# Kernel optimization log

Measured on AMD Instinct MI355X. Metric: run time of the kernel, lower is better.

Reference implementation:

```python
import jax, jax.numpy as jnp
import numpy as np
import itertools

VOXEL_SIZE = np.array([0.05, 0.05, 0.1], np.float32)   # xyz, from cfg.voxel_size
GRID_OFFSET = np.array([0.0, -40.0, -3.0], np.float32)  # xyz, cfg.grid_bounds[:3]
BN_EPS = 1e-3

# ---------------- rulebook construction (numpy, mirrors spconv indice pairs) ----------------

def _enc(c, shape):
    Z, Y, X = shape
    c = c.astype(np.int64)
    return ((c[:, 0] * Z + c[:, 1]) * Y + c[:, 2]) * X + c[:, 3]

def _lookup(sk, order, q):
    pos = np.clip(np.searchsorted(sk, q), 0, len(sk) - 1)
    return np.where((q >= 0) & (sk[pos] == q), order[pos], -1).astype(np.int32)

def _subm_rulebook(coords, shape):
    # submanifold conv k=3, pad=1: output sites == input sites; neighbor = out + (k-1)
    keys = _enc(coords, shape)
    order = np.argsort(keys).astype(np.int32)
    sk = keys[order]
    dims = np.array(shape)
    rows = []
    for off in itertools.product((-1, 0, 1), repeat=3):
        nb = coords[:, 1:] + np.array(off)
        inb = ((nb >= 0) & (nb < dims)).all(1)
        full = np.concatenate([coords[:, :1], nb], 1)
        q = np.where(inb, _enc(full, shape), -1)
        rows.append(_lookup(sk, order, q))
    return np.stack(rows)  # [27, N] input index or -1

def _strided_rulebook(coords, shape_in, ksize, stride, pad):
    # regular sparse conv: out active = any site receiving a contribution; in = out*s - p + k
    ksize = np.array(ksize); stride = np.array(stride); pad = np.array(pad)
    shape_out = tuple((((np.array(shape_in) + 2 * pad - ksize) // stride) + 1).tolist())
    keys = _enc(coords, shape_in)
    order = np.argsort(keys).astype(np.int32)
    sk = keys[order]
    cand = []
    for k in itertools.product(*[range(int(x)) for x in ksize]):
        num = coords[:, 1:] + pad - np.array(k)
        ok = (num % stride == 0).all(1)
        o = num // stride
        ok &= (o >= 0).all(1) & (o < np.array(shape_out)).all(1)
        cand.append(np.concatenate([coords[ok, :1], o[ok]], 1))
    out_coords = np.unique(np.concatenate(cand, 0), axis=0).astype(np.int32)
    dims_in = np.array(shape_in)
    rows = []
    for k in itertools.product(*[range(int(x)) for x in ksize]):
        ic = out_coords[:, 1:] * stride - pad + np.array(k)
        inb = ((ic >= 0) & (ic < dims_in)).all(1)
        full = np.concatenate([out_coords[:, :1], ic], 1)
        q = np.where(inb, _enc(full, shape_in), -1)
        rows.append(_lookup(sk, order, q))
    return out_coords, np.stack(rows), shape_out

# ---------------- inputs ----------------

def setup_inputs() -> dict:
    rng = np.random.default_rng(0)
    B, NPB = 2, 8000
    shape0 = (41, 1600, 1280)
    parts = []
    for b in range(B):
        c = np.stack([rng.integers(0, shape0[0], 4 * NPB),
                      rng.integers(0, shape0[1], 4 * NPB),
                      rng.integers(0, shape0[2], 4 * NPB)], 1)
        c = np.unique(c, axis=0)[:NPB]
        parts.append(np.concatenate([np.full((len(c), 1), b), c], 1))
    coords0 = np.concatenate(parts, 0).astype(np.int32)

    rb0 = _subm_rulebook(coords0, shape0)
    coords1, rbc1, shape1 = _strided_rulebook(coords0, shape0, (3, 3, 3), (2, 2, 2), (1, 1, 1))
    rb1 = _subm_rulebook(coords1, shape1)
    coords2, rbc2, shape2 = _strided_rulebook(coords1, shape1, (3, 3, 3), (2, 2, 2), (1, 1, 1))
    rb2 = _subm_rulebook(coords2, shape2)
    coords3, rbc3, shape3 = _strided_rulebook(coords2, shape2, (3, 3, 3), (2, 2, 2), (0, 1, 1))
    rb3 = _subm_rulebook(coords3, shape3)
    coords4, rbc4, shape4 = _strided_rulebook(coords3, shape3, (3, 1, 1), (2, 1, 1), (0, 0, 0))

    def w(*s):
        return jnp.asarray((rng.standard_normal(s) * 0.1).astype(np.float32))

    inp = {"features": jnp.asarray(rng.standard_normal((len(coords0), 4)).astype(np.float32))}
    specs = [("1a", 27, 4, 16), ("1b", 27, 16, 16), ("1c", 27, 16, 32),
             ("2a", 27, 32, 32), ("2b", 27, 32, 32), ("2c", 27, 32, 64),
             ("3a", 27, 64, 64), ("3b", 27, 64, 64), ("3c", 27, 64, 64), ("3d", 27, 64, 64),
             ("4a", 27, 64, 64), ("4b", 27, 64, 64), ("4c", 27, 64, 64), ("4d", 3, 64, 64)]
    for name, K, ci, co in specs:
        inp["w" + name] = w(K, ci, co)
        inp["g" + name] = jnp.asarray((np.abs(rng.standard_normal(co)) + 0.5).astype(np.float32))
        inp["b" + name] = jnp.asarray((rng.standard_normal(co) * 0.1).astype(np.float32))
    inp.update(coordinates=jnp.asarray(coords0), coords1=jnp.asarray(coords1),
               coords2=jnp.asarray(coords2), coords3=jnp.asarray(coords3),
               rb0=jnp.asarray(rb0), rbc1=jnp.asarray(rbc1), rb1=jnp.asarray(rb1),
               rbc2=jnp.asarray(rbc2), rb2=jnp.asarray(rb2), rbc3=jnp.asarray(rbc3),
               rb3=jnp.asarray(rb3), rbc4=jnp.asarray(rbc4), batch_size=B)
    return inp

# ---------------- forward math ----------------

def _sconv(feat, rb, W):
    # gather-GEMM-scatter: rb[k,n] = input row feeding output n via kernel offset k (-1 = none)
    out = jnp.zeros((rb.shape[1], W.shape[2]), feat.dtype)
    for k in range(W.shape[0]):
        idx = rb[k]
        g = jnp.where(idx[:, None] >= 0, feat[jnp.clip(idx, 0)], 0.0)
        out = out + g @ W[k]
    return out

def _bn_relu(x, g, b):
    # BatchNorm1d in training mode over active voxels (biased var), eps=1e-3, then ReLU
    m = jnp.mean(x, 0)
    v = jnp.mean(jnp.square(x - m), 0)
    return jax.nn.relu((x - m) * (g / jnp.sqrt(v + BN_EPS)) + b)

def reference(features, w1a, g1a, b1a, w1b, g1b, b1b, w1c, g1c, b1c,
              w2a, g2a, b2a, w2b, g2b, b2b, w2c, g2c, b2c,
              w3a, g3a, b3a, w3b, g3b, b3b, w3c, g3c, b3c, w3d, g3d, b3d,
              w4a, g4a, b4a, w4b, g4b, b4b, w4c, g4c, b4c, w4d, g4d, b4d,
              coordinates, coords1, coords2, coords3,
              rb0, rbc1, rb1, rbc2, rb2, rbc3, rb3, rbc4, batch_size):
    f0 = features
    h = _bn_relu(_sconv(f0, rb0, w1a), g1a, b1a)
    h = _bn_relu(_sconv(h, rb0, w1b), g1b, b1b)
    f1 = _bn_relu(_sconv(h, rbc1, w1c), g1c, b1c)
    h = _bn_relu(_sconv(f1, rb1, w2a), g2a, b2a)
    h = _bn_relu(_sconv(h, rb1, w2b), g2b, b2b)
    f2 = _bn_relu(_sconv(h, rbc2, w2c), g2c, b2c)
    h = _bn_relu(_sconv(f2, rb2, w3a), g3a, b3a)
    h = _bn_relu(_sconv(h, rb2, w3b), g3b, b3b)
    h = _bn_relu(_sconv(h, rb2, w3c), g3c, b3c)
    f3 = _bn_relu(_sconv(h, rbc3, w3d), g3d, b3d)
    h = _bn_relu(_sconv(f3, rb3, w4a), g4a, b4a)
    h = _bn_relu(_sconv(h, rb3, w4b), g4b, b4b)
    h = _bn_relu(_sconv(h, rb3, w4c), g4c, b4c)
    f4 = _bn_relu(_sconv(h, rbc4, w4d), g4d, b4d)

    vs = jnp.asarray(VOXEL_SIZE)
    off = jnp.asarray(GRID_OFFSET)
    def to_global(stride, c):
        # indices are (b,z,y,x); flip -> (x,y,z,b); take xyz
        return jnp.flip(c, 1)[:, :3].astype(jnp.float32) * (vs * stride) + off
    xyz0 = to_global(1, coordinates)
    xyz1 = to_global(2, coords1)
    xyz2 = to_global(4, coords2)
    xyz3 = to_global(8, coords3)
    return (xyz0, f0, xyz1, f1, xyz2, f2, xyz3, f3, f4)
```

## Files before the change

### kernel.cpp

```cpp
#include <hip/hip_runtime.h>

#define BN_EPS 1e-3f
#define NREP 16

typedef __attribute__((ext_vector_type(8))) short short8;
typedef __attribute__((ext_vector_type(4))) float float4v;

__device__ __forceinline__ short f2bf(float f) {
    unsigned u = __float_as_uint(f);
    unsigned r = (u + 0x7FFFu + ((u >> 16) & 1u)) >> 16;
    return (short)r;
}

template <int N>
__device__ __forceinline__ void waitcnt_vm() {
    __builtin_amdgcn_s_waitcnt(0xF70 | (N & 15) | ((N >> 4) << 14));
}

__device__ __forceinline__ void wave_barrier() { asm volatile("s_barrier" ::: "memory"); }

__device__ __forceinline__ void dma16(const short* g, short* l) {
    __builtin_amdgcn_global_load_lds((const __attribute__((address_space(1))) void*)g,
                                     (__attribute__((address_space(3))) void*)l, 16, 0, 0);
}


__global__ __launch_bounds__(256) void zero_kernel(float* p, int n) {
    int i = blockIdx.x * 256 + threadIdx.x;
    if (i < n) p[i] = 0.f;
}

__global__ __launch_bounds__(256) void copy_kernel(const float* __restrict__ in,
                                                   float* __restrict__ out, int n) {
    int i = blockIdx.x * 256 + threadIdx.x;
    if (i < n) out[i] = in[i];
}

__global__ __launch_bounds__(256) void zero_rows_kernel(short* a, short* b, long maxN) {
    int t = threadIdx.x;
    if (t < 32) a[maxN * 32 + t] = 0;
    else if (t < 96) a[maxN * 64 + (t - 32)] = 0;
    else if (t < 128) b[maxN * 32 + (t - 96)] = 0;
    else if (t < 192) b[maxN * 64 + (t - 128)] = 0;
}

__global__ __launch_bounds__(256) void xyz_kernel(const int* __restrict__ coords,
                                                  float* __restrict__ out, int N,
                                                  float sx, float sy, float sz) {
    int n = blockIdx.x * 256 + threadIdx.x;
    if (n >= N) return;
    int4 c = ((const int4*)coords)[n];
    out[n * 3 + 0] = c.w * sx;
    out[n * 3 + 1] = c.z * sy - 40.0f;
    out[n * 3 + 2] = c.y * sz - 3.0f;
}

__global__ __launch_bounds__(256) void convert_f0(const float* __restrict__ f,
                                                  short* __restrict__ dst, int N) {
    int i = blockIdx.x * 256 + threadIdx.x;
    if (i >= N * 32) return;
    int c = i & 31, n = i >> 5;
    dst[i] = (c < 4) ? f2bf(f[n * 4 + c]) : (short)0;
}

struct PrepAll {
    const float* src[14];
    short* dst[14];
    int CI[14];
    int CO[14];
    int CHP[14];
    int cum[15];
};

__global__ __launch_bounds__(256) void prep_all_kernel(PrepAll d) {
    int i = blockIdx.x * 256 + threadIdx.x;
    if (i >= d.cum[14]) return;
    int l = 0;
    while (l < 13 && i >= d.cum[l + 1]) ++l;
    int f = i - d.cum[l];
    int CO = d.CO[l], CI = d.CI[l];
    int NCH = d.CHP[l] / 32, CT = CO / 16;
    int e = f & 7;
    int u = f >> 3;
    int l16 = u & 15;
    int q = (u >> 4) & 3;
    int u2 = u >> 6;
    int t = u2 % CT;
    int c = (u2 / CT) % NCH;
    int k = u2 / (CT * NCH);
    int ci = c * 32 + q * 8 + e;
    int co = t * 16 + l16;
    float v = (ci < CI) ? d.src[l][((size_t)k * CI + ci) * CO + co] : 0.f;
    d.dst[l][f] = f2bf(v);
}

struct ASet {
    short8 v0, v1, v2, v3;
};

template <int CHP, int CO, int K>
__global__ __launch_bounds__(256, 4) void sconv_hyb(const short* __restrict__ feat,
                                                    const int* __restrict__ rb,
                                                    const short* __restrict__ Wt,
                                                    float* __restrict__ out,
                                                    float* __restrict__ stats, int N, int zrow) {
    constexpr int NCH = CHP / 32;
    constexpr int CT = CO / 16;
    constexpr int BTILE = CO * CHP;
    constexpr int NB = BTILE / 512;
    constexpr int A = 2 * NCH;
    constexpr int ROWS = 128;

    __shared__ __align__(16) short ldsB[3 * BTILE];
    __shared__ int sIdx[K * ROWS];
    __shared__ int sFlag[K];
    __shared__ int sKl[K];
    __shared__ int sKn;

    const int tid = threadIdx.x;
    const int w = tid >> 6;
    const int lane = tid & 63;
    const int quad = lane >> 4;
    const int l16 = lane & 15;
    const int m0 = blockIdx.x * ROWS;

    if (tid < K) sFlag[tid] = 0;
    __syncthreads();
    for (int e = tid; e < K * ROWS; e += 256) {
        int r = m0 + (e & (ROWS - 1));
        int v = (r < N) ? rb[(size_t)(e >> 7) * N + r] : -1;
        sIdx[e] = v;
        if (v >= 0) sFlag[e >> 7] = 1;
    }
    __syncthreads();
    if (w == 0) {
        int f = (lane < K) ? sFlag[lane] : 0;
        unsigned long long m = __ballot(f != 0);
        if (f) sKl[__popcll(m & ((1ull << lane) - 1ull))] = lane;
        if (lane == 0) sKn = (int)__popcll(m);
    }
    __syncthreads();
    const int nk = sKn;

    const short* fquad = feat + quad * 8;

    auto issueB = [&](int kp, int slot) {
        const short* wk = Wt + (size_t)kp * BTILE + lane * 8;
        short* bb = ldsB + slot * BTILE;
#pragma unroll
        for (int jj = 0; jj < (NB + 3) / 4; ++jj) {
            int j = jj * 4 + w;
            if (j < NB) dma16(wk + j * 512, bb + j * 512);
        }
    };
    auto issueA = [&](int kp) {
        ASet s;
        int i0 = sIdx[kp * ROWS + w * 32 + l16];
        int i1 = sIdx[kp * ROWS + w * 32 + 16 + l16];
        const short* p0 = fquad + (size_t)(i0 < 0 ? zrow : i0) * CHP;
        const short* p1 = fquad + (size_t)(i1 < 0 ? zrow : i1) * CHP;
        s.v0 = *(const short8*)p0;
        s.v2 = *(const short8*)p1;
        if constexpr (NCH == 2) {
            s.v1 = *(const short8*)(p0 + 32);
            s.v3 = *(const short8*)(p1 + 32);
        } else {
            s.v1 = (short8)0;
            s.v3 = (short8)0;
        }
        return s;
    };

    float4v acc[2][CT];
#pragma unroll
    for (int mt = 0; mt < 2; ++mt)
#pragma unroll
        for (int t = 0; t < CT; ++t) acc[mt][t] = (float4v)0.f;

    constexpr int BW0 = NB / 4 + ((NB % 4) > 0 ? 1 : 0);
    constexpr int BW1 = NB / 4 + ((NB % 4) > 1 ? 1 : 0);
    constexpr int BW2 = NB / 4 + ((NB % 4) > 2 ? 1 : 0);
    constexpr int BW3 = NB / 4;

    ASet sA{}, sB{}, sC{};
    if (nk > 0) {
        issueB(sKl[0], 0);
        sA = issueA(sKl[0]);
    }
    if (nk > 1) {
        issueB(sKl[1], 1);
        sB = issueA(sKl[1]);
    }

    int slotRd = 0, slotWr = 2;
    for (int i = 0; i < nk; ++i) {
        if (i < nk - 1) {
            if (w == 0) waitcnt_vm<BW0 + A>();
            else if (w == 1) waitcnt_vm<BW1 + A>();
            else if (w == 2) waitcnt_vm<BW2 + A>();
            else waitcnt_vm<BW3 + A>();
        } else {
            waitcnt_vm<0>();
        }
        __builtin_amdgcn_sched_barrier(0);
        wave_barrier();
        if (i + 2 < nk) {
            issueB(sKl[i + 2], slotWr);
            sC = issueA(sKl[i + 2]);
        }
        const short* bb = ldsB + slotRd * BTILE;
#pragma unroll
        for (int c = 0; c < NCH; ++c) {
#pragma unroll
            for (int t = 0; t < CT; ++t) {
                short8 bf = *(const short8*)(bb + ((c * CT + t) * 64 + quad * 16 + l16) * 8);
#pragma unroll
                for (int mt = 0; mt < 2; ++mt) {
                    short8 af = (mt == 0) ? ((c == 0) ? sA.v0 : sA.v1)
                                          : ((c == 0) ? sA.v2 : sA.v3);
                    acc[mt][t] = __builtin_amdgcn_mfma_f32_16x16x32_bf16(af, bf, acc[mt][t], 0,
                                                                         0, 0);
                }
            }
        }
        sA = sB;
        sB = sC;
        slotRd = (slotRd == 2) ? 0 : slotRd + 1;
        slotWr = (slotWr == 2) ? 0 : slotWr + 1;
    }

#pragma unroll
    for (int mt = 0; mt < 2; ++mt)
#pragma unroll
        for (int t = 0; t < CT; ++t) {
            int col = t * 16 + l16;
#pragma unroll
            for (int r = 0; r < 4; ++r) {
                int orow = m0 + w * 32 + mt * 16 + quad * 4 + r;
                if (orow < N) out[(size_t)orow * CO + col] = acc[mt][t][r];
            }
        }

    __syncthreads();
    float* red = (float*)ldsB;
#pragma unroll
    for (int t = 0; t < CT; ++t) {
        float s = 0.f, ss = 0.f;
#pragma unroll
        for (int mt = 0; mt < 2; ++mt)
#pragma unroll
            for (int r = 0; r < 4; ++r) {
                float v = acc[mt][t][r];
                s += v;
                ss += v * v;
            }
        s += __shfl_xor(s, 16);
        s += __shfl_xor(s, 32);
        ss += __shfl_xor(ss, 16);
        ss += __shfl_xor(ss, 32);
        if (lane < 16) {
            red[w * 2 * CO + t * 16 + lane] = s;
            red[w * 2 * CO + CO + t * 16 + lane] = ss;
        }
    }
    __syncthreads();
    if (tid < 2 * CO) {
        float v = red[tid] + red[2 * CO + tid] + red[4 * CO + tid] + red[6 * CO + tid];
        float* st = stats + (size_t)(blockIdx.x & (NREP - 1)) * 128;
        atomicAdd(&st[(tid < CO) ? tid : (64 + tid - CO)], v);
    }
}

template <int COUT, int CHPN, bool F32OUT, bool BFOUT>
__global__ __launch_bounds__(256) void bn_apply(const float* __restrict__ x,
                                                const float* __restrict__ stats,
                                                const float* __restrict__ g,
                                                const float* __restrict__ b,
                                                float* __restrict__ fout,
                                                short* __restrict__ bfout, int N) {
    constexpr int CW = BFOUT ? CHPN : COUT;
    __shared__ float ssc[COUT];
    __shared__ float ssh[COUT];
    int tid = threadIdx.x;
    if (tid < COUT) {
        float s = 0.f, q = 0.f;
#pragma unroll
        for (int r = 0; r < NREP; ++r) {
            s += stats[r * 128 + tid];
            q += stats[r * 128 + 64 + tid];
        }
        float inv = 1.0f / (float)N;
        float m = s * inv;
        float v = q * inv - m * m;
        float sc = g[tid] / sqrtf(v + BN_EPS);
        ssc[tid] = sc;
        ssh[tid] = b[tid] - m * sc;
    }
    __syncthreads();
    long i = (long)blockIdx.x * 256 + tid;
    if (i >= (long)N * CW) return;
    int c = (int)(i % CW);
    long n = i / CW;
    float y = 0.f;
    if (c < COUT) {
        y = fmaxf(x[n * COUT + c] * ssc[c] + ssh[c], 0.f);
        if (F32OUT) __builtin_nontemporal_store(y, &fout[n * COUT + c]);
    }
    if (BFOUT) bfout[n * CHPN + c] = f2bf(y);
}


template <int CHP, int CO, int K>
static void conv(const short* fin, const int* rb, const short* wt, float* preact, float* stats,
                 int N, int zrow, hipStream_t stream) {
    dim3 grid((N + 127) / 128);
    hipLaunchKernelGGL((sconv_hyb<CHP, CO, K>), grid, dim3(256), 0, stream, fin, rb, wt, preact,
                       stats, N, zrow);
}

template <int COUT, int CHPN, bool F32OUT, bool BFOUT>
static void apply(const float* preact, const float* stats, const float* g, const float* b,
                  float* fout, short* bfout, int N, hipStream_t stream) {
    constexpr int CW = BFOUT ? CHPN : COUT;
    int blocks = (int)(((long)N * CW + 255) / 256);
    hipLaunchKernelGGL((bn_apply<COUT, CHPN, F32OUT, BFOUT>), dim3(blocks), dim3(256), 0, stream,
                       preact, stats, g, b, fout, bfout, N);
}

extern "C" void kernel_launch(void* const* d_in, const int* in_sizes, int n_in, void* d_out,
                              int out_size, void* d_ws, size_t ws_size, hipStream_t stream) {
    const float* features = (const float*)d_in[0];
    const float* W[14];
    const float* G[14];
    const float* Bb[14];
    for (int i = 0; i < 14; ++i) {
        W[i] = (const float*)d_in[1 + 3 * i];
        G[i] = (const float*)d_in[2 + 3 * i];
        Bb[i] = (const float*)d_in[3 + 3 * i];
    }
    const int* coords0 = (const int*)d_in[43];
    const int* coords1 = (const int*)d_in[44];
    const int* coords2 = (const int*)d_in[45];
    const int* coords3 = (const int*)d_in[46];
    const int* rb0 = (const int*)d_in[47];
    const int* rbc1 = (const int*)d_in[48];
    const int* rb1 = (const int*)d_in[49];
    const int* rbc2 = (const int*)d_in[50];
    const int* rb2 = (const int*)d_in[51];
    const int* rbc3 = (const int*)d_in[52];
    const int* rb3 = (const int*)d_in[53];
    const int* rbc4 = (const int*)d_in[54];

    const int N0 = in_sizes[0] / 4;
    const int N1 = in_sizes[44] / 4;
    const int N2 = in_sizes[45] / 4;
    const int N3 = in_sizes[46] / 4;
    const int N4 = in_sizes[54] / 3;

    float* out = (float*)d_out;
    long off = 0;
    float* xyz0 = out + off; off += (long)N0 * 3;
    float* f0   = out + off; off += (long)N0 * 4;
    float* xyz1 = out + off; off += (long)N1 * 3;
    float* f1   = out + off; off += (long)N1 * 32;
    float* xyz2 = out + off; off += (long)N2 * 3;
    float* f2   = out + off; off += (long)N2 * 64;
    float* xyz3 = out + off; off += (long)N3 * 3;
    float* f3   = out + off; off += (long)N3 * 64;
    float* f4   = out + off;

    long maxN = N0;
    if (N1 > maxN) maxN = N1;
    if (N2 > maxN) maxN = N2;
    if (N3 > maxN) maxN = N3;
    if (N4 > maxN) maxN = N4;
    const int zrow = (int)maxN;

    float* preact = (float*)d_ws;
    float* statsBase = preact + (size_t)maxN * 64;
    short* bfA = (short*)(statsBase + 14 * NREP * 128);
    short* bfB = bfA + (size_t)(maxN + 1) * 64;
    short* wtBase = bfB + (size_t)(maxN + 1) * 64;

    static const int KK[14] = {27, 27, 27, 27, 27, 27, 27, 27, 27, 27, 27, 27, 27, 3};
    static const int CI[14] = {4, 16, 16, 32, 32, 32, 64, 64, 64, 64, 64, 64, 64, 64};
    static const int CO[14] = {16, 16, 32, 32, 32, 64, 64, 64, 64, 64, 64, 64, 64, 64};
    short* WT[14];
    PrepAll pd;
    {
        size_t o = 0;
        int cum = 0;
        for (int l = 0; l < 14; ++l) {
            WT[l] = wtBase + o;
            int chp = CI[l] <= 32 ? 32 : 64;
            pd.src[l] = W[l];
            pd.dst[l] = WT[l];
            pd.CI[l] = CI[l];
            pd.CO[l] = CO[l];
            pd.CHP[l] = chp;
            pd.cum[l] = cum;
            cum += KK[l] * CO[l] * chp;
            o += (size_t)KK[l] * CO[l] * chp;
        }
        pd.cum[14] = cum;
    }

    int nstats = 14 * NREP * 128;
    hipLaunchKernelGGL(zero_kernel, dim3((nstats + 255) / 256), dim3(256), 0, stream, statsBase,
                       nstats);
    hipLaunchKernelGGL(zero_rows_kernel, dim3(1), dim3(256), 0, stream, bfA, bfB, maxN);
    hipLaunchKernelGGL(prep_all_kernel, dim3((pd.cum[14] + 255) / 256), dim3(256), 0, stream, pd);

    hipLaunchKernelGGL(copy_kernel, dim3((N0 * 4 + 255) / 256), dim3(256), 0, stream, features, f0,
                       N0 * 4);
    hipLaunchKernelGGL(xyz_kernel, dim3((N0 + 255) / 256), dim3(256), 0, stream, coords0, xyz0, N0,
                       0.05f, 0.05f, 0.1f);
    hipLaunchKernelGGL(xyz_kernel, dim3((N1 + 255) / 256), dim3(256), 0, stream, coords1, xyz1, N1,
                       0.1f, 0.1f, 0.2f);
    hipLaunchKernelGGL(xyz_kernel, dim3((N2 + 255) / 256), dim3(256), 0, stream, coords2, xyz2, N2,
                       0.2f, 0.2f, 0.4f);
    hipLaunchKernelGGL(xyz_kernel, dim3((N3 + 255) / 256), dim3(256), 0, stream, coords3, xyz3, N3,
                       0.4f, 0.4f, 0.8f);
    hipLaunchKernelGGL(convert_f0, dim3((N0 * 32 + 255) / 256), dim3(256), 0, stream, features,
                       bfA, N0);

    float* st = statsBase;
#define STAT(l) (st + (size_t)(l)*NREP * 128)

    conv<32, 16, 27>(bfA, rb0, WT[0], preact, STAT(0), N0, zrow, stream);
    apply<16, 32, false, true>(preact, STAT(0), G[0], Bb[0], nullptr, bfB, N0, stream);
    conv<32, 16, 27>(bfB, rb0, WT[1], preact, STAT(1), N0, zrow, stream);
    apply<16, 32, false, true>(preact, STAT(1), G[1], Bb[1], nullptr, bfA, N0, stream);
    conv<32, 32, 27>(bfA, rbc1, WT[2], preact, STAT(2), N1, zrow, stream);
    apply<32, 32, true, true>(preact, STAT(2), G[2], Bb[2], f1, bfB, N1, stream);

    conv<32, 32, 27>(bfB, rb1, WT[3], preact, STAT(3), N1, zrow, stream);
    apply<32, 32, false, true>(preact, STAT(3), G[3], Bb[3], nullptr, bfA, N1, stream);
    conv<32, 32, 27>(bfA, rb1, WT[4], preact, STAT(4), N1, zrow, stream);
    apply<32, 32, false, true>(preact, STAT(4), G[4], Bb[4], nullptr, bfB, N1, stream);
    conv<32, 64, 27>(bfB, rbc2, WT[5], preact, STAT(5), N2, zrow, stream);
    apply<64, 64, true, true>(preact, STAT(5), G[5], Bb[5], f2, bfA, N2, stream);

    conv<64, 64, 27>(bfA, rb2, WT[6], preact, STAT(6), N2, zrow, stream);
    apply<64, 64, false, true>(preact, STAT(6), G[6], Bb[6], nullptr, bfB, N2, stream);
    conv<64, 64, 27>(bfB, rb2, WT[7], preact, STAT(7), N2, zrow, stream);
    apply<64, 64, false, true>(preact, STAT(7), G[7], Bb[7], nullptr, bfA, N2, stream);
    conv<64, 64, 27>(bfA, rb2, WT[8], preact, STAT(8), N2, zrow, stream);
    apply<64, 64, false, true>(preact, STAT(8), G[8], Bb[8], nullptr, bfB, N2, stream);
    conv<64, 64, 27>(bfB, rbc3, WT[9], preact, STAT(9), N3, zrow, stream);
    apply<64, 64, true, true>(preact, STAT(9), G[9], Bb[9], f3, bfA, N3, stream);

    conv<64, 64, 27>(bfA, rb3, WT[10], preact, STAT(10), N3, zrow, stream);
    apply<64, 64, false, true>(preact, STAT(10), G[10], Bb[10], nullptr, bfB, N3, stream);
    conv<64, 64, 27>(bfB, rb3, WT[11], preact, STAT(11), N3, zrow, stream);
    apply<64, 64, false, true>(preact, STAT(11), G[11], Bb[11], nullptr, bfA, N3, stream);
    conv<64, 64, 27>(bfA, rb3, WT[12], preact, STAT(12), N3, zrow, stream);
    apply<64, 64, false, true>(preact, STAT(12), G[12], Bb[12], nullptr, bfB, N3, stream);
    conv<64, 64, 3>(bfB, rbc4, WT[13], preact, STAT(13), N4, zrow, stream);
    apply<64, 64, true, false>(preact, STAT(13), G[13], Bb[13], f4, nullptr, N4, stream);
#undef STAT
}
```

Before: 733.1 us.

## Split sparse conv kernel offsets across grid y and reduce partials separately

The conv kernel now splits the 27 kernel offsets into 4 groups using blockIdx.y. Each group writes its own partial output buffer. A new reduce_stats kernel sums the partials into a combined buffer and computes the BN sum and sum-of-squares statistics, which the conv epilogue no longer does. This raises parallelism for small-N layers and lowers per-block LDS index storage, but it adds extra global memory traffic for the partials, an extra launch per layer, and more reloading of the same rows.

```diff
diff --git a/kernel.cpp b/kernel.cpp
--- a/kernel.cpp
+++ b/kernel.cpp
@@ -98,12 +98,12 @@
     short8 v0, v1, v2, v3;
 };
 
-template <int CHP, int CO, int K>
+template <int CHP, int CO, int KS>
 __global__ __launch_bounds__(256, 4) void sconv_hyb(const short* __restrict__ feat,
                                                     const int* __restrict__ rb,
                                                     const short* __restrict__ Wt,
-                                                    float* __restrict__ out,
-                                                    float* __restrict__ stats, int N, int zrow) {
+                                                    float* __restrict__ parts, long pstride,
+                                                    int N, int zrow, int Ktot) {
     constexpr int NCH = CHP / 32;
     constexpr int CT = CO / 16;
     constexpr int BTILE = CO * CHP;
@@ -112,9 +112,9 @@
     constexpr int ROWS = 128;
 
     __shared__ __align__(16) short ldsB[3 * BTILE];
-    __shared__ int sIdx[K * ROWS];
-    __shared__ int sFlag[K];
-    __shared__ int sKl[K];
+    __shared__ int sIdx[KS * ROWS];
+    __shared__ int sFlag[KS];
+    __shared__ int sKl[KS];
     __shared__ int sKn;
 
     const int tid = threadIdx.x;
@@ -123,18 +123,22 @@
     const int quad = lane >> 4;
     const int l16 = lane & 15;
     const int m0 = blockIdx.x * ROWS;
-
-    if (tid < K) sFlag[tid] = 0;
+    const int kbase = blockIdx.y * KS;
+    int kn = Ktot - kbase;
+    if (kn > KS) kn = KS;
+    float* __restrict__ out = parts + (size_t)blockIdx.y * pstride;
+
+    if (tid < KS) sFlag[tid] = 0;
     __syncthreads();
-    for (int e = tid; e < K * ROWS; e += 256) {
+    for (int e = tid; e < kn * ROWS; e += 256) {
         int r = m0 + (e & (ROWS - 1));
-        int v = (r < N) ? rb[(size_t)(e >> 7) * N + r] : -1;
+        int v = (r < N) ? rb[(size_t)(kbase + (e >> 7)) * N + r] : -1;
         sIdx[e] = v;
         if (v >= 0) sFlag[e >> 7] = 1;
     }
     __syncthreads();
     if (w == 0) {
-        int f = (lane < K) ? sFlag[lane] : 0;
+        int f = (lane < kn) ? sFlag[lane] : 0;
         unsigned long long m = __ballot(f != 0);
         if (f) sKl[__popcll(m & ((1ull << lane) - 1ull))] = lane;
         if (lane == 0) sKn = (int)__popcll(m);
@@ -144,8 +148,8 @@
 
     const short* fquad = feat + quad * 8;
 
-    auto issueB = [&](int kp, int slot) {
-        const short* wk = Wt + (size_t)kp * BTILE + lane * 8;
+    auto issueB = [&](int kg, int slot) {
+        const short* wk = Wt + (size_t)kg * BTILE + lane * 8;
         short* bb = ldsB + slot * BTILE;
 #pragma unroll
         for (int jj = 0; jj < (NB + 3) / 4; ++jj) {
@@ -184,11 +188,11 @@
 
     ASet sA{}, sB{}, sC{};
     if (nk > 0) {
-        issueB(sKl[0], 0);
+        issueB(kbase + sKl[0], 0);
         sA = issueA(sKl[0]);
     }
     if (nk > 1) {
-        issueB(sKl[1], 1);
+        issueB(kbase + sKl[1], 1);
         sB = issueA(sKl[1]);
     }
 
@@ -205,7 +209,7 @@
         __builtin_amdgcn_sched_barrier(0);
         wave_barrier();
         if (i + 2 < nk) {
-            issueB(sKl[i + 2], slotWr);
+            issueB(kbase + sKl[i + 2], slotWr);
             sC = issueA(sKl[i + 2]);
         }
         const short* bb = ldsB + slotRd * BTILE;
@@ -240,34 +244,50 @@
                 if (orow < N) out[(size_t)orow * CO + col] = acc[mt][t][r];
             }
         }
-
+}
+
+template <int COUT, int SPLITS>
+__global__ __launch_bounds__(256) void reduce_stats(const float* __restrict__ parts, long pstride,
+                                                    float* __restrict__ comb,
+                                                    float* __restrict__ stats, int N) {
+    constexpr int RPP = 256 / COUT;
+    constexpr int NPASS = 8;
+    int tid = threadIdx.x;
+    int c = tid & (COUT - 1);
+    int rl = tid / COUT;
+    long base = (long)blockIdx.x * (NPASS * RPP) + rl;
+    float s = 0.f, q = 0.f;
+#pragma unroll
+    for (int p = 0; p < NPASS; ++p) {
+        long r = base + (long)p * RPP;
+        if (r < N) {
+            float v = parts[r * COUT + c];
+            if (SPLITS > 1) {
+#pragma unroll
+                for (int sp = 1; sp < SPLITS; ++sp) v += parts[(size_t)sp * pstride + r * COUT + c];
+                comb[r * COUT + c] = v;
+            }
+            s += v;
+            q += v * v;
+        }
+    }
+    __shared__ float sS[256];
+    __shared__ float sQ[256];
+    sS[tid] = s;
+    sQ[tid] = q;
     __syncthreads();
-    float* red = (float*)ldsB;
-#pragma unroll
-    for (int t = 0; t < CT; ++t) {
-        float s = 0.f, ss = 0.f;
-#pragma unroll
-        for (int mt = 0; mt < 2; ++mt)
-#pragma unroll
-            for (int r = 0; r < 4; ++r) {
-                float v = acc[mt][t][r];
-                s += v;
-                ss += v * v;
-            }
-        s += __shfl_xor(s, 16);
-        s += __shfl_xor(s, 32);
-        ss += __shfl_xor(ss, 16);
-        ss += __shfl_xor(ss, 32);
-        if (lane < 16) {
-            red[w * 2 * CO + t * 16 + lane] = s;
-            red[w * 2 * CO + CO + t * 16 + lane] = ss;
-        }
-    }
-    __syncthreads();
-    if (tid < 2 * CO) {
-        float v = red[tid] + red[2 * CO + tid] + red[4 * CO + tid] + red[6 * CO + tid];
+#pragma unroll
+    for (int off = 128; off >= COUT; off >>= 1) {
+        if (tid < off) {
+            sS[tid] += sS[tid + off];
+            sQ[tid] += sQ[tid + off];
+        }
+        __syncthreads();
+    }
+    if (tid < COUT) {
         float* st = stats + (size_t)(blockIdx.x & (NREP - 1)) * 128;
-        atomicAdd(&st[(tid < CO) ? tid : (64 + tid - CO)], v);
+        atomicAdd(&st[tid], sS[tid]);
+        atomicAdd(&st[64 + tid], sQ[tid]);
     }
 }
 
@@ -310,12 +330,22 @@
 }
 
 
-template <int CHP, int CO, int K>
-static void conv(const short* fin, const int* rb, const short* wt, float* preact, float* stats,
+template <int CHP, int CO, int K, int SPLITS>
+static void conv(const short* fin, const int* rb, const short* wt, float* parts, long pstride,
                  int N, int zrow, hipStream_t stream) {
-    dim3 grid((N + 127) / 128);
-    hipLaunchKernelGGL((sconv_hyb<CHP, CO, K>), grid, dim3(256), 0, stream, fin, rb, wt, preact,
-                       stats, N, zrow);
+    constexpr int KS = (K + SPLITS - 1) / SPLITS;
+    dim3 grid((N + 127) / 128, SPLITS);
+    hipLaunchKernelGGL((sconv_hyb<CHP, CO, KS>), grid, dim3(256), 0, stream, fin, rb, wt, parts,
+                       pstride, N, zrow, K);
+}
+
+template <int COUT, int SPLITS>
+static void reduce(const float* parts, long pstride, float* comb, float* stats, int N,
+                   hipStream_t stream) {
+    constexpr int RPB = 8 * (256 / COUT);
+    int blocks = (N + RPB - 1) / RPB;
+    hipLaunchKernelGGL((reduce_stats<COUT, SPLITS>), dim3(blocks), dim3(256), 0, stream, parts,
+                       pstride, comb, stats, N);
 }
 
 template <int COUT, int CHPN, bool F32OUT, bool BFOUT>
@@ -375,9 +405,11 @@
     if (N3 > maxN) maxN = N3;
     if (N4 > maxN) maxN = N4;
     const int zrow = (int)maxN;
-
-    float* preact = (float*)d_ws;
-    float* statsBase = preact + (size_t)maxN * 64;
+    const long pstrideF = (long)maxN * 64;
+
+    float* comb = (float*)d_ws;
+    float* parts = comb + pstrideF;
+    float* statsBase = parts + 4 * pstrideF;
     short* bfA = (short*)(statsBase + 14 * NREP * 128);
     short* bfB = bfA + (size_t)(maxN + 1) * 64;
     short* wtBase = bfB + (size_t)(maxN + 1) * 64;
@@ -426,37 +458,31 @@
 
     float* st = statsBase;
 #define STAT(l) (st + (size_t)(l)*NREP * 128)
-
-    conv<32, 16, 27>(bfA, rb0, WT[0], preact, STAT(0), N0, zrow, stream);
-    apply<16, 32, false, true>(preact, STAT(0), G[0], Bb[0], nullptr, bfB, N0, stream);
-    conv<32, 16, 27>(bfB, rb0, WT[1], preact, STAT(1), N0, zrow, stream);
-    apply<16, 32, false, true>(preact, STAT(1), G[1], Bb[1], nullptr, bfA, N0, stream);
-    conv<32, 32, 27>(bfA, rbc1, WT[2], preact, STAT(2), N1, zrow, stream);
-    apply<32, 32, true, true>(preact, STAT(2), G[2], Bb[2], f1, bfB, N1, stream);
-
-    conv<32, 32, 27>(bfB, rb1, WT[3], preact, STAT(3), N1, zrow, stream);
-    apply<32, 32, false, true>(preact, STAT(3), G[3], Bb[3], nullptr, bfA, N1, stream);
-    conv<32, 32, 27>(bfA, rb1, WT[4], preact, STAT(4), N1, zrow, stream);
-    apply<32, 32, false, true>(preact, STAT(4), G[4], Bb[4], nullptr, bfB, N1, stream);
-    conv<32, 64, 27>(bfB, rbc2, WT[5], preact, STAT(5), N2, zrow, stream);
-    apply<64, 64, true, true>(preact, STAT(5), G[5], Bb[5], f2, bfA, N2, stream);
-
-    conv<64, 64, 27>(bfA, rb2, WT[6], preact, STAT(6), N2, zrow, stream);
-    apply<64, 64, false, true>(preact, STAT(6), G[6], Bb[6], nullptr, bfB, N2, stream);
-    conv<64, 64, 27>(bfB, rb2, WT[7], preact, STAT(7), N2, zrow, stream);
-    apply<64, 64, false, true>(preact, STAT(7), G[7], Bb[7], nullptr, bfA, N2, stream);
-    conv<64, 64, 27>(bfA, rb2, WT[8], preact, STAT(8), N2, zrow, stream);
-    apply<64, 64, false, true>(preact, STAT(8), G[8], Bb[8], nullptr, bfB, N2, stream);
-    conv<64, 64, 27>(bfB, rbc3, WT[9], preact, STAT(9), N3, zrow, stream);
-    apply<64, 64, true, true>(preact, STAT(9), G[9], Bb[9], f3, bfA, N3, stream);
-
-    conv<64, 64, 27>(bfA, rb3, WT[10], preact, STAT(10), N3, zrow, stream);
-    apply<64, 64, false, true>(preact, STAT(10), G[10], Bb[10], nullptr, bfB, N3, stream);
-    conv<64, 64, 27>(bfB, rb3, WT[11], preact, STAT(11), N3, zrow, stream);
-    apply<64, 64, false, true>(preact, STAT(11), G[11], Bb[11], nullptr, bfA, N3, stream);
-    conv<64, 64, 27>(bfA, rb3, WT[12], preact, STAT(12), N3, zrow, stream);
-    apply<64, 64, false, true>(preact, STAT(12), G[12], Bb[12], nullptr, bfB, N3, stream);
-    conv<64, 64, 3>(bfB, rbc4, WT[13], preact, STAT(13), N4, zrow, stream);
-    apply<64, 64, true, false>(preact, STAT(13), G[13], Bb[13], f4, nullptr, N4, stream);
+#define LAYER(CHP, CHPO, COx, K, SPL, fin, rbp, l, N, fo, bfo, F32O, BFO)                         \
+    do {                                                                                          \
+        conv<CHP, COx, K, SPL>(fin, rbp, WT[l], parts, pstrideF, N, zrow, stream);                \
+        reduce<COx, SPL>(parts, pstrideF, comb, STAT(l), N, stream);                              \
+        apply<COx, CHPO, F32O, BFO>((SPL > 1) ? comb : parts, STAT(l), G[l], Bb[l], fo, bfo, N,   \
+                                    stream);                                                      \
+    } while (0)
+
+    LAYER(32, 32, 16, 27, 4, bfA, rb0, 0, N0, nullptr, bfB, false, true);
+    LAYER(32, 32, 16, 27, 4, bfB, rb0, 1, N0, nullptr, bfA, false, true);
+    LAYER(32, 32, 32, 27, 4, bfA, rbc1, 2, N1, f1, bfB, true, true);
+
+    LAYER(32, 32, 32, 27, 4, bfB, rb1, 3, N1, nullptr, bfA, false, true);
+    LAYER(32, 32, 32, 27, 4, bfA, rb1, 4, N1, nullptr, bfB, false, true);
+    LAYER(32, 64, 64, 27, 4, bfB, rbc2, 5, N2, f2, bfA, true, true);
+
+    LAYER(64, 64, 64, 27, 4, bfA, rb2, 6, N2, nullptr, bfB, false, true);
+    LAYER(64, 64, 64, 27, 4, bfB, rb2, 7, N2, nullptr, bfA, false, true);
+    LAYER(64, 64, 64, 27, 4, bfA, rb2, 8, N2, nullptr, bfB, false, true);
+    LAYER(64, 64, 64, 27, 4, bfB, rbc3, 9, N3, f3, bfA, true, true);
+
+    LAYER(64, 64, 64, 27, 4, bfA, rb3, 10, N3, nullptr, bfB, false, true);
+    LAYER(64, 64, 64, 27, 4, bfB, rb3, 11, N3, nullptr, bfA, false, true);
+    LAYER(64, 64, 64, 27, 4, bfA, rb3, 12, N3, nullptr, bfB, false, true);
+    LAYER(64, 64, 64, 3, 1, bfB, rbc4, 13, N4, f4, nullptr, true, false);
+#undef LAYER
 #undef STAT
 }
```

Result: slower. 828.7 us (+13.0%).

## Fuse sparse conv and batchnorm apply into persistent cooperative kernel with grid sync

Applied to the files above, without the earlier changes.

Merges each conv kernel and its separate BN-apply kernel into one cooperative persistent kernel. Tiles accumulate BN statistics, the grid synchronises, then each block applies scale/shift/ReLU straight from its accumulators and writes the bf16/f32 outputs. When there are more tiles than resident blocks, it falls back to storing preactivations and re-reading them after the sync. This removes one launch and the fp32 preact round trip per layer, at the cost of a grid-wide barrier and a cooperative-launch retry loop.

```diff
diff --git a/kernel.cpp b/kernel.cpp
--- a/kernel.cpp
+++ b/kernel.cpp
@@ -1,4 +1,7 @@
 #include <hip/hip_runtime.h>
+#include <hip/hip_cooperative_groups.h>
+
+namespace cg = cooperative_groups;
 
 #define BN_EPS 1e-3f
 #define NREP 16
@@ -98,12 +101,12 @@
     short8 v0, v1, v2, v3;
 };
 
-template <int CHP, int CO, int K>
-__global__ __launch_bounds__(256, 4) void sconv_hyb(const short* __restrict__ feat,
-                                                    const int* __restrict__ rb,
-                                                    const short* __restrict__ Wt,
-                                                    float* __restrict__ out,
-                                                    float* __restrict__ stats, int N, int zrow) {
+template <int CHP, int CO, int K, bool F32OUT, bool BFOUT, int CHPO>
+__global__ __launch_bounds__(256, 4) void sconv_pers(
+    const short* __restrict__ feat, const int* __restrict__ rb, const short* __restrict__ Wt,
+    const float* __restrict__ g, const float* __restrict__ b, float* __restrict__ stats,
+    float* __restrict__ preact, float* __restrict__ fout, short* __restrict__ bfout, int N,
+    int zrow, int tiles) {
     constexpr int NCH = CHP / 32;
     constexpr int CT = CO / 16;
     constexpr int BTILE = CO * CHP;
@@ -122,26 +125,7 @@
     const int lane = tid & 63;
     const int quad = lane >> 4;
     const int l16 = lane & 15;
-    const int m0 = blockIdx.x * ROWS;
-
-    if (tid < K) sFlag[tid] = 0;
-    __syncthreads();
-    for (int e = tid; e < K * ROWS; e += 256) {
-        int r = m0 + (e & (ROWS - 1));
-        int v = (r < N) ? rb[(size_t)(e >> 7) * N + r] : -1;
-        sIdx[e] = v;
-        if (v >= 0) sFlag[e >> 7] = 1;
-    }
-    __syncthreads();
-    if (w == 0) {
-        int f = (lane < K) ? sFlag[lane] : 0;
-        unsigned long long m = __ballot(f != 0);
-        if (f) sKl[__popcll(m & ((1ull << lane) - 1ull))] = lane;
-        if (lane == 0) sKn = (int)__popcll(m);
-    }
-    __syncthreads();
-    const int nk = sKn;
-
+    const bool multi = tiles > (int)gridDim.x;
     const short* fquad = feat + quad * 8;
 
     auto issueB = [&](int kp, int slot) {
@@ -171,160 +155,229 @@
         return s;
     };
 
-    float4v acc[2][CT];
-#pragma unroll
-    for (int mt = 0; mt < 2; ++mt)
-#pragma unroll
-        for (int t = 0; t < CT; ++t) acc[mt][t] = (float4v)0.f;
-
     constexpr int BW0 = NB / 4 + ((NB % 4) > 0 ? 1 : 0);
     constexpr int BW1 = NB / 4 + ((NB % 4) > 1 ? 1 : 0);
     constexpr int BW2 = NB / 4 + ((NB % 4) > 2 ? 1 : 0);
     constexpr int BW3 = NB / 4;
 
-    ASet sA{}, sB{}, sC{};
-    if (nk > 0) {
-        issueB(sKl[0], 0);
-        sA = issueA(sKl[0]);
-    }
-    if (nk > 1) {
-        issueB(sKl[1], 1);
-        sB = issueA(sKl[1]);
-    }
-
-    int slotRd = 0, slotWr = 2;
-    for (int i = 0; i < nk; ++i) {
-        if (i < nk - 1) {
-            if (w == 0) waitcnt_vm<BW0 + A>();
-            else if (w == 1) waitcnt_vm<BW1 + A>();
-            else if (w == 2) waitcnt_vm<BW2 + A>();
-            else waitcnt_vm<BW3 + A>();
-        } else {
-            waitcnt_vm<0>();
-        }
-        __builtin_amdgcn_sched_barrier(0);
-        wave_barrier();
-        if (i + 2 < nk) {
-            issueB(sKl[i + 2], slotWr);
-            sC = issueA(sKl[i + 2]);
-        }
-        const short* bb = ldsB + slotRd * BTILE;
-#pragma unroll
-        for (int c = 0; c < NCH; ++c) {
-#pragma unroll
-            for (int t = 0; t < CT; ++t) {
-                short8 bf = *(const short8*)(bb + ((c * CT + t) * 64 + quad * 16 + l16) * 8);
-#pragma unroll
-                for (int mt = 0; mt < 2; ++mt) {
-                    short8 af = (mt == 0) ? ((c == 0) ? sA.v0 : sA.v1)
-                                          : ((c == 0) ? sA.v2 : sA.v3);
-                    acc[mt][t] = __builtin_amdgcn_mfma_f32_16x16x32_bf16(af, bf, acc[mt][t], 0,
-                                                                         0, 0);
+    float4v acc[2][CT];
+
+    for (int tile = blockIdx.x; tile < tiles; tile += gridDim.x) {
+        const int m0 = tile * ROWS;
+
+        if (tid < K) sFlag[tid] = 0;
+        __syncthreads();
+        for (int e = tid; e < K * ROWS; e += 256) {
+            int r = m0 + (e & (ROWS - 1));
+            int v = (r < N) ? rb[(size_t)(e >> 7) * N + r] : -1;
+            sIdx[e] = v;
+            if (v >= 0) sFlag[e >> 7] = 1;
+        }
+        __syncthreads();
+        if (w == 0) {
+            int f = (lane < K) ? sFlag[lane] : 0;
+            unsigned long long m = __ballot(f != 0);
+            if (f) sKl[__popcll(m & ((1ull << lane) - 1ull))] = lane;
+            if (lane == 0) sKn = (int)__popcll(m);
+        }
+        __syncthreads();
+        const int nk = sKn;
+
+#pragma unroll
+        for (int mt = 0; mt < 2; ++mt)
+#pragma unroll
+            for (int t = 0; t < CT; ++t) acc[mt][t] = (float4v)0.f;
+
+        ASet sA{}, sB{}, sC{};
+        if (nk > 0) {
+            issueB(sKl[0], 0);
+            sA = issueA(sKl[0]);
+        }
+        if (nk > 1) {
+            issueB(sKl[1], 1);
+            sB = issueA(sKl[1]);
+        }
+
+        int slotRd = 0, slotWr = 2;
+        for (int i = 0; i < nk; ++i) {
+            if (i < nk - 1) {
+                if (w == 0) waitcnt_vm<BW0 + A>();
+                else if (w == 1) waitcnt_vm<BW1 + A>();
+                else if (w == 2) waitcnt_vm<BW2 + A>();
+                else waitcnt_vm<BW3 + A>();
+            } else {
+                waitcnt_vm<0>();
+            }
+            __builtin_amdgcn_sched_barrier(0);
+            wave_barrier();
+            if (i + 2 < nk) {
+                issueB(sKl[i + 2], slotWr);
+                sC = issueA(sKl[i + 2]);
+            }
+            const short* bb = ldsB + slotRd * BTILE;
+#pragma unroll
+            for (int c = 0; c < NCH; ++c) {
+#pragma unroll
+                for (int t = 0; t < CT; ++t) {
+                    short8 bf = *(const short8*)(bb + ((c * CT + t) * 64 + quad * 16 + l16) * 8);
+#pragma unroll
+                    for (int mt = 0; mt < 2; ++mt) {
+                        short8 af = (mt == 0) ? ((c == 0) ? sA.v0 : sA.v1)
+                                              : ((c == 0) ? sA.v2 : sA.v3);
+                        acc[mt][t] =
+                            __builtin_amdgcn_mfma_f32_16x16x32_bf16(af, bf, acc[mt][t], 0, 0, 0);
+                    }
                 }
             }
-        }
-        sA = sB;
-        sB = sC;
-        slotRd = (slotRd == 2) ? 0 : slotRd + 1;
-        slotWr = (slotWr == 2) ? 0 : slotWr + 1;
-    }
-
-#pragma unroll
-    for (int mt = 0; mt < 2; ++mt)
+            sA = sB;
+            sB = sC;
+            slotRd = (slotRd == 2) ? 0 : slotRd + 1;
+            slotWr = (slotWr == 2) ? 0 : slotWr + 1;
+        }
+
+        __syncthreads();
+        float* red = (float*)ldsB;
 #pragma unroll
         for (int t = 0; t < CT; ++t) {
-            int col = t * 16 + l16;
-#pragma unroll
-            for (int r = 0; r < 4; ++r) {
-                int orow = m0 + w * 32 + mt * 16 + quad * 4 + r;
-                if (orow < N) out[(size_t)orow * CO + col] = acc[mt][t][r];
+            float s = 0.f, ss = 0.f;
+#pragma unroll
+            for (int mt = 0; mt < 2; ++mt)
+#pragma unroll
+                for (int r = 0; r < 4; ++r) {
+                    int orow = m0 + w * 32 + mt * 16 + quad * 4 + r;
+                    float v = (orow < N) ? acc[mt][t][r] : 0.f;
+                    s += v;
+                    ss += v * v;
+                }
+            s += __shfl_xor(s, 16);
+            s += __shfl_xor(s, 32);
+            ss += __shfl_xor(ss, 16);
+            ss += __shfl_xor(ss, 32);
+            if (lane < 16) {
+                red[w * 2 * CO + t * 16 + lane] = s;
+                red[w * 2 * CO + CO + t * 16 + lane] = ss;
             }
         }
-
+        __syncthreads();
+        if (tid < 2 * CO) {
+            float v = red[tid] + red[2 * CO + tid] + red[4 * CO + tid] + red[6 * CO + tid];
+            float* st = stats + (size_t)(tile & (NREP - 1)) * 128;
+            atomicAdd(&st[(tid < CO) ? tid : (64 + tid - CO)], v);
+        }
+
+        if (multi) {
+#pragma unroll
+            for (int mt = 0; mt < 2; ++mt)
+#pragma unroll
+                for (int t = 0; t < CT; ++t) {
+                    int col = t * 16 + l16;
+#pragma unroll
+                    for (int r = 0; r < 4; ++r) {
+                        int orow = m0 + w * 32 + mt * 16 + quad * 4 + r;
+                        if (orow < N) preact[(size_t)orow * CO + col] = acc[mt][t][r];
+                    }
+                }
+        }
+    }
+
+    cg::this_grid().sync();
+
+    float* red = (float*)ldsB;
     __syncthreads();
-    float* red = (float*)ldsB;
-#pragma unroll
-    for (int t = 0; t < CT; ++t) {
-        float s = 0.f, ss = 0.f;
-#pragma unroll
-        for (int mt = 0; mt < 2; ++mt)
-#pragma unroll
-            for (int r = 0; r < 4; ++r) {
-                float v = acc[mt][t][r];
-                s += v;
-                ss += v * v;
-            }
-        s += __shfl_xor(s, 16);
-        s += __shfl_xor(s, 32);
-        ss += __shfl_xor(ss, 16);
-        ss += __shfl_xor(ss, 32);
-        if (lane < 16) {
-            red[w * 2 * CO + t * 16 + lane] = s;
-            red[w * 2 * CO + CO + t * 16 + lane] = ss;
-        }
-    }
-    __syncthreads();
-    if (tid < 2 * CO) {
-        float v = red[tid] + red[2 * CO + tid] + red[4 * CO + tid] + red[6 * CO + tid];
-        float* st = stats + (size_t)(blockIdx.x & (NREP - 1)) * 128;
-        atomicAdd(&st[(tid < CO) ? tid : (64 + tid - CO)], v);
-    }
-}
-
-template <int COUT, int CHPN, bool F32OUT, bool BFOUT>
-__global__ __launch_bounds__(256) void bn_apply(const float* __restrict__ x,
-                                                const float* __restrict__ stats,
-                                                const float* __restrict__ g,
-                                                const float* __restrict__ b,
-                                                float* __restrict__ fout,
-                                                short* __restrict__ bfout, int N) {
-    constexpr int CW = BFOUT ? CHPN : COUT;
-    __shared__ float ssc[COUT];
-    __shared__ float ssh[COUT];
-    int tid = threadIdx.x;
-    if (tid < COUT) {
+    if (tid < CO) {
         float s = 0.f, q = 0.f;
 #pragma unroll
-        for (int r = 0; r < NREP; ++r) {
-            s += stats[r * 128 + tid];
-            q += stats[r * 128 + 64 + tid];
+        for (int r2 = 0; r2 < NREP; ++r2) {
+            s += __hip_atomic_load(&stats[r2 * 128 + tid], __ATOMIC_RELAXED,
+                                   __HIP_MEMORY_SCOPE_AGENT);
+            q += __hip_atomic_load(&stats[r2 * 128 + 64 + tid], __ATOMIC_RELAXED,
+                                   __HIP_MEMORY_SCOPE_AGENT);
         }
         float inv = 1.0f / (float)N;
         float m = s * inv;
         float v = q * inv - m * m;
         float sc = g[tid] / sqrtf(v + BN_EPS);
-        ssc[tid] = sc;
-        ssh[tid] = b[tid] - m * sc;
+        red[tid] = sc;
+        red[CO + tid] = b[tid] - m * sc;
     }
     __syncthreads();
-    long i = (long)blockIdx.x * 256 + tid;
-    if (i >= (long)N * CW) return;
-    int c = (int)(i % CW);
-    long n = i / CW;
-    float y = 0.f;
-    if (c < COUT) {
-        y = fmaxf(x[n * COUT + c] * ssc[c] + ssh[c], 0.f);
-        if (F32OUT) __builtin_nontemporal_store(y, &fout[n * COUT + c]);
-    }
-    if (BFOUT) bfout[n * CHPN + c] = f2bf(y);
-}
-
-
-template <int CHP, int CO, int K>
-static void conv(const short* fin, const int* rb, const short* wt, float* preact, float* stats,
-                 int N, int zrow, hipStream_t stream) {
-    dim3 grid((N + 127) / 128);
-    hipLaunchKernelGGL((sconv_hyb<CHP, CO, K>), grid, dim3(256), 0, stream, fin, rb, wt, preact,
-                       stats, N, zrow);
-}
-
-template <int COUT, int CHPN, bool F32OUT, bool BFOUT>
-static void apply(const float* preact, const float* stats, const float* g, const float* b,
-                  float* fout, short* bfout, int N, hipStream_t stream) {
-    constexpr int CW = BFOUT ? CHPN : COUT;
-    int blocks = (int)(((long)N * CW + 255) / 256);
-    hipLaunchKernelGGL((bn_apply<COUT, CHPN, F32OUT, BFOUT>), dim3(blocks), dim3(256), 0, stream,
-                       preact, stats, g, b, fout, bfout, N);
+
+    if (!multi) {
+        const int m0 = blockIdx.x * ROWS;
+#pragma unroll
+        for (int mt = 0; mt < 2; ++mt)
+#pragma unroll
+            for (int t = 0; t < CT; ++t) {
+                int col = t * 16 + l16;
+                float sc = red[col];
+                float sh = red[CO + col];
+#pragma unroll
+                for (int r = 0; r < 4; ++r) {
+                    int orow = m0 + w * 32 + mt * 16 + quad * 4 + r;
+                    if (orow < N) {
+                        float y = fmaxf(acc[mt][t][r] * sc + sh, 0.f);
+                        if constexpr (F32OUT) fout[(size_t)orow * CO + col] = y;
+                        if constexpr (BFOUT) {
+                            bfout[(size_t)orow * CHPO + col] = f2bf(y);
+                            if constexpr (CHPO > CO)
+                                bfout[(size_t)orow * CHPO + CO + l16] = 0;
+                        }
+                    }
+                }
+            }
+    } else {
+        for (int tile = blockIdx.x; tile < tiles; tile += gridDim.x) {
+            const int m0 = tile * ROWS;
+#pragma unroll
+            for (int mt = 0; mt < 2; ++mt)
+#pragma unroll
+                for (int t = 0; t < CT; ++t) {
+                    int col = t * 16 + l16;
+                    float sc = red[col];
+                    float sh = red[CO + col];
+#pragma unroll
+                    for (int r = 0; r < 4; ++r) {
+                        int orow = m0 + w * 32 + mt * 16 + quad * 4 + r;
+                        if (orow < N) {
+                            float y = fmaxf(preact[(size_t)orow * CO + col] * sc + sh, 0.f);
+                            if constexpr (F32OUT) fout[(size_t)orow * CO + col] = y;
+                            if constexpr (BFOUT) {
+                                bfout[(size_t)orow * CHPO + col] = f2bf(y);
+                                if constexpr (CHPO > CO)
+                                    bfout[(size_t)orow * CHPO + CO + l16] = 0;
+                            }
+                        }
+                    }
+                }
+        }
+    }
+}
+
+
+template <int CHP, int CO, int K, bool F32OUT, bool BFOUT, int CHPO>
+static void layer(const short* fin, const int* rb, const short* wt, const float* g,
+                  const float* b, float* stats, float* preact, float* fout, short* bfout, int N,
+                  int zrow, hipStream_t stream) {
+    auto kfn = sconv_pers<CHP, CO, K, F32OUT, BFOUT, CHPO>;
+    static int maxB = 0;
+    if (maxB == 0) {
+        int m = 0;
+        if (hipOccupancyMaxActiveBlocksPerMultiprocessor(&m, kfn, 256, 0) != hipSuccess || m < 1)
+            m = 1;
+        maxB = m;
+    }
+    int tiles = (N + 127) / 128;
+    int cap = maxB * 256;
+    int grid = tiles < cap ? tiles : cap;
+    void* args[] = {(void*)&fin,   (void*)&rb,   (void*)&wt,    (void*)&g,   (void*)&b,
+                    (void*)&stats, (void*)&preact, (void*)&fout, (void*)&bfout, (void*)&N,
+                    (void*)&zrow,  (void*)&tiles};
+    while (grid >= 1) {
+        hipError_t e = hipLaunchCooperativeKernel(reinterpret_cast<void*>(kfn), dim3(grid),
+                                                  dim3(256), args, 0, stream);
+        if (e == hipSuccess) break;
+        grid >>= 1;
+    }
 }
 
 extern "C" void kernel_launch(void* const* d_in, const int* in_sizes, int n_in, void* d_out,
@@ -427,36 +480,36 @@
     float* st = statsBase;
 #define STAT(l) (st + (size_t)(l)*NREP * 128)
 
-    conv<32, 16, 27>(bfA, rb0, WT[0], preact, STAT(0), N0, zrow, stream);
-    apply<16, 32, false, true>(preact, STAT(0), G[0], Bb[0], nullptr, bfB, N0, stream);
-    conv<32, 16, 27>(bfB, rb0, WT[1], preact, STAT(1), N0, zrow, stream);
-    apply<16, 32, false, true>(preact, STAT(1), G[1], Bb[1], nullptr, bfA, N0, stream);
-    conv<32, 32, 27>(bfA, rbc1, WT[2], preact, STAT(2), N1, zrow, stream);
-    apply<32, 32, true, true>(preact, STAT(2), G[2], Bb[2], f1, bfB, N1, stream);
-
-    conv<32, 32, 27>(bfB, rb1, WT[3], preact, STAT(3), N1, zrow, stream);
-    apply<32, 32, false, true>(preact, STAT(3), G[3], Bb[3], nullptr, bfA, N1, stream);
-    conv<32, 32, 27>(bfA, rb1, WT[4], preact, STAT(4), N1, zrow, stream);
-    apply<32, 32, false, true>(preact, STAT(4), G[4], Bb[4], nullptr, bfB, N1, stream);
-    conv<32, 64, 27>(bfB, rbc2, WT[5], preact, STAT(5), N2, zrow, stream);
-    apply<64, 64, true, true>(preact, STAT(5), G[5], Bb[5], f2, bfA, N2, stream);
-
-    conv<64, 64, 27>(bfA, rb2, WT[6], preact, STAT(6), N2, zrow, stream);
-    apply<64, 64, false, true>(preact, STAT(6), G[6], Bb[6], nullptr, bfB, N2, stream);
-    conv<64, 64, 27>(bfB, rb2, WT[7], preact, STAT(7), N2, zrow, stream);
-    apply<64, 64, false, true>(preact, STAT(7), G[7], Bb[7], nullptr, bfA, N2, stream);
-    conv<64, 64, 27>(bfA, rb2, WT[8], preact, STAT(8), N2, zrow, stream);
-    apply<64, 64, false, true>(preact, STAT(8), G[8], Bb[8], nullptr, bfB, N2, stream);
-    conv<64, 64, 27>(bfB, rbc3, WT[9], preact, STAT(9), N3, zrow, stream);
-    apply<64, 64, true, true>(preact, STAT(9), G[9], Bb[9], f3, bfA, N3, stream);
-
-    conv<64, 64, 27>(bfA, rb3, WT[10], preact, STAT(10), N3, zrow, stream);
-    apply<64, 64, false, true>(preact, STAT(10), G[10], Bb[10], nullptr, bfB, N3, stream);
-    conv<64, 64, 27>(bfB, rb3, WT[11], preact, STAT(11), N3, zrow, stream);
-    apply<64, 64, false, true>(preact, STAT(11), G[11], Bb[11], nullptr, bfA, N3, stream);
-    conv<64, 64, 27>(bfA, rb3, WT[12], preact, STAT(12), N3, zrow, stream);
-    apply<64, 64, false, true>(preact, STAT(12), G[12], Bb[12], nullptr, bfB, N3, stream);
-    conv<64, 64, 3>(bfB, rbc4, WT[13], preact, STAT(13), N4, zrow, stream);
-    apply<64, 64, true, false>(preact, STAT(13), G[13], Bb[13], f4, nullptr, N4, stream);
+    layer<32, 16, 27, false, true, 32>(bfA, rb0, WT[0], G[0], Bb[0], STAT(0), preact, nullptr, bfB,
+                                       N0, zrow, stream);
+    layer<32, 16, 27, false, true, 32>(bfB, rb0, WT[1], G[1], Bb[1], STAT(1), preact, nullptr, bfA,
+                                       N0, zrow, stream);
+    layer<32, 32, 27, true, true, 32>(bfA, rbc1, WT[2], G[2], Bb[2], STAT(2), preact, f1, bfB, N1,
+                                      zrow, stream);
+
+    layer<32, 32, 27, false, true, 32>(bfB, rb1, WT[3], G[3], Bb[3], STAT(3), preact, nullptr, bfA,
+                                       N1, zrow, stream);
+    layer<32, 32, 27, false, true, 32>(bfA, rb1, WT[4], G[4], Bb[4], STAT(4), preact, nullptr, bfB,
+                                       N1, zrow, stream);
+    layer<32, 64, 27, true, true, 64>(bfB, rbc2, WT[5], G[5], Bb[5], STAT(5), preact, f2, bfA, N2,
+                                      zrow, stream);
+
+    layer<64, 64, 27, false, true, 64>(bfA, rb2, WT[6], G[6], Bb[6], STAT(6), preact, nullptr, bfB,
+                                       N2, zrow, stream);
+    layer<64, 64, 27, false, true, 64>(bfB, rb2, WT[7], G[7], Bb[7], STAT(7), preact, nullptr, bfA,
+                                       N2, zrow, stream);
+    layer<64, 64, 27, false, true, 64>(bfA, rb2, WT[8], G[8], Bb[8], STAT(8), preact, nullptr, bfB,
+                                       N2, zrow, stream);
+    layer<64, 64, 27, true, true, 64>(bfB, rbc3, WT[9], G[9], Bb[9], STAT(9), preact, f3, bfA, N3,
+                                      zrow, stream);
+
+    layer<64, 64, 27, false, true, 64>(bfA, rb3, WT[10], G[10], Bb[10], STAT(10), preact, nullptr,
+                                       bfB, N3, zrow, stream);
+    layer<64, 64, 27, false, true, 64>(bfB, rb3, WT[11], G[11], Bb[11], STAT(11), preact, nullptr,
+                                       bfA, N3, zrow, stream);
+    layer<64, 64, 27, false, true, 64>(bfA, rb3, WT[12], G[12], Bb[12], STAT(12), preact, nullptr,
+                                       bfB, N3, zrow, stream);
+    layer<64, 64, 3, true, false, 64>(bfB, rbc4, WT[13], G[13], Bb[13], STAT(13), preact, f4,
+                                      nullptr, N4, zrow, stream);
 #undef STAT
 }
```

After: 1.704 ms. +132.4%, slower.
